# Kernel optimization log

Hardware: AMD Instinct MI355X
Metric: run time of the kernel (lower is better)

The kernel has to match this reference:

```python
import jax, jax.numpy as jnp
import numpy as np

H = 256
NUM_CONVS = 4
NUM_GRAPHS = 1024
N_PER_GRAPH = 32
ORDER = 3
NUM_TYPES = 22  # len(utils.BOND_TYPES)
NUM_NOISE_LEVEL = 50
ANNEAL_POWER = 2.0


def _build_graph():
    # Chain molecules extended to order-3 neighbors (mimics extend_graph on a path graph):
    # for |i-j| in [1,ORDER]: edge_order=|i-j|, edge_type = bond type if order 1 else NUM_TYPES+order-1.
    n = N_PER_GRAPH
    i, j = np.meshgrid(np.arange(n), np.arange(n), indexing='ij')
    dist = np.abs(i - j)
    mask = (dist >= 1) & (dist <= ORDER)
    src_l, dst_l, eo = i[mask], j[mask], dist[mask]
    offs = np.arange(NUM_GRAPHS)[:, None] * n
    src = (src_l[None, :] + offs).reshape(-1)
    dst = (dst_l[None, :] + offs).reshape(-1)
    edge_order = np.tile(eo, NUM_GRAPHS)
    rng = np.random.default_rng(0)
    bond_t = rng.integers(1, 5, size=edge_order.shape)
    edge_type = np.where(edge_order == 1, bond_t, NUM_TYPES + edge_order - 1)
    node2graph = np.repeat(np.arange(NUM_GRAPHS), n)
    return src, dst, edge_type, node2graph


def setup_inputs() -> dict:
    key = jax.random.key(0)
    ks = jax.random.split(key, 24)
    src, dst, edge_type, node2graph = _build_graph()
    N, E = node2graph.shape[0], src.shape[0]
    w = lambda k, s: (jax.random.normal(k, s, jnp.float32) * 0.05)
    sigmas = jnp.asarray(np.exp(np.linspace(np.log(10.0), np.log(0.01), NUM_NOISE_LEVEL)), dtype=jnp.float32)
    return {
        'atom_type': jnp.asarray(np.random.default_rng(1).integers(0, 100, N), jnp.int32),
        'edge_index': jnp.asarray(np.stack([src, dst]), jnp.int32),
        'edge_type': jnp.asarray(edge_type, jnp.int32),
        'node2graph': jnp.asarray(node2graph, jnp.int32),
        'noise_level': jax.random.randint(ks[0], (NUM_GRAPHS,), 0, NUM_NOISE_LEVEL, jnp.int32),
        'pos': jax.random.normal(ks[1], (N, 3), jnp.float32) * 3.0,
        'd_noise': jax.random.normal(ks[2], (E, 1), jnp.float32),
        'sigmas': sigmas,
        'node_emb': w(ks[3], (100, H)), 'edge_emb': w(ks[4], (100, H)),
        'in_W1': w(ks[5], (1, H)), 'in_b1': w(ks[6], (H,)),
        'in_W2': w(ks[7], (H, H)), 'in_b2': w(ks[8], (H,)),
        'gin_W1': w(ks[9], (NUM_CONVS, H, H)), 'gin_b1': w(ks[10], (NUM_CONVS, H)),
        'gin_W2': w(ks[11], (NUM_CONVS, H, H)), 'gin_b2': w(ks[12], (NUM_CONVS, H)),
        'out_W1': w(ks[13], (2 * H, H)), 'out_b1': w(ks[14], (H,)),
        'out_W2': w(ks[15], (H, H // 2)), 'out_b2': w(ks[16], (H // 2,)),
        'out_W3': w(ks[17], (H // 2, 1)), 'out_b3': w(ks[18], (1,)),
    }


def reference(atom_type, edge_index, edge_type, node2graph, noise_level,
              pos, d_noise, sigmas, node_emb, edge_emb,
              in_W1, in_b1, in_W2, in_b2,
              gin_W1, gin_b1, gin_W2, gin_b2,
              out_W1, out_b1, out_W2, out_b2, out_W3, out_b3):
    N = pos.shape[0]
    G = noise_level.shape[0]
    row, col = edge_index[0], edge_index[1]
    edge2graph = node2graph[row]                                  # [E]
    d = jnp.linalg.norm(pos[row] - pos[col], axis=-1, keepdims=True)  # [E,1]
    used_sigmas = sigmas[noise_level][edge2graph][:, None]        # [E,1]
    perturbed_d = d + d_noise * used_sigmas
    target = -(perturbed_d - d) / used_sigmas ** 2
    # embeddings + input MLP (Linear-relu-Linear)
    node_attr = node_emb[atom_type]                               # [N,H]
    d_emb = jax.nn.relu(perturbed_d @ in_W1 + in_b1) @ in_W2 + in_b2
    edge_attr = d_emb * edge_emb[edge_type]                       # [E,H]
    # GIN with GINE convs: agg = sum_j relu(x_j + e_ij); out = MLP(x + agg); relu between convs; residual
    x = node_attr
    n_convs = gin_W1.shape[0]
    for k in range(n_convs):
        msg = jax.nn.relu(x[row] + edge_attr)                     # [E,H]
        agg = jax.ops.segment_sum(msg, col, num_segments=N)       # [N,H]
        h = jax.nn.relu((x + agg) @ gin_W1[k] + gin_b1[k]) @ gin_W2[k] + gin_b2[k]
        if k < n_convs - 1:
            h = jax.nn.relu(h)
        x = h + x  # short_cut
    # edge score head
    feat = jnp.concatenate([x[row] * x[col], edge_attr], axis=-1)  # [E,2H]
    s = jax.nn.relu(feat @ out_W1 + out_b1)
    s = jax.nn.relu(s @ out_W2 + out_b2)
    s = s @ out_W3 + out_b3                                       # [E,1]
    scores = (s / used_sigmas).reshape(-1)
    t = target.reshape(-1)
    loss_e = 0.5 * (scores - t) ** 2 * used_sigmas.reshape(-1) ** ANNEAL_POWER
    return jax.ops.segment_sum(loss_e, edge2graph, num_segments=G)  # [G]
```

## Files before the change

### kernel.cpp

```cpp
#include <hip/hip_runtime.h>
#include <math.h>

typedef unsigned int u32;
typedef __attribute__((ext_vector_type(8))) short bf16x8;
typedef __attribute__((ext_vector_type(4))) float f32x4;

#define MFMA16(a,b,c) __builtin_amdgcn_mfma_f32_16x16x32_bf16(a,b,c,0,0,0)

__device__ inline u32 bf16r(float x){
  u32 u = __float_as_uint(x);
  return (u + 0x7fffu + ((u >> 16) & 1u)) >> 16;
}
__device__ inline u32 pack2(float a, float b){ return bf16r(a) | (bf16r(b) << 16); }
__device__ inline uint4 pack8(const float* f){
  uint4 v; v.x = pack2(f[0],f[1]); v.y = pack2(f[2],f[3]);
  v.z = pack2(f[4],f[5]); v.w = pack2(f[6],f[7]); return v;
}
__device__ inline float bf2f(short s){ return __uint_as_float(((u32)(unsigned short)s) << 16); }

__device__ __forceinline__ void gload_lds16(const void* g, void* l){
  __builtin_amdgcn_global_load_lds((const __attribute__((address_space(1))) unsigned int*)g,
                                   (__attribute__((address_space(3))) unsigned int*)l,
                                   16, 0, 0);
}

__device__ __forceinline__ int frag_off(int f, int quad){
  return (f>>1)*64 + (f&1)*32 + ((quad ^ ((f>>1)&3))*8);
}

__device__ __forceinline__ int xg2(int g, int r){ return g ^ ((r ^ (g>>1)) & 7); }

__global__ void k_cvtAll(const float* __restrict__ inW2, const float* __restrict__ gW1,
                         const float* __restrict__ gW2, const float* __restrict__ oW1,
                         const float* __restrict__ oW2,
                         short* __restrict__ w2t, short* __restrict__ gw1t,
                         short* __restrict__ gw2t, short* __restrict__ ow1t,
                         short* __restrict__ ow2t){
  int gidx = blockIdx.x*256 + threadIdx.x;
  const float* src; short* dst; int t, K8, Nf;
  if (gidx < 8192)      { src = inW2; dst = w2t; t = gidx; K8 = 32; Nf = 256; }
  else if (gidx < 40960){ int r = gidx-8192;  int c = r>>13; t = r&8191;
                          src = gW1 + (size_t)c*65536; dst = gw1t + (size_t)c*65536; K8 = 32; Nf = 256; }
  else if (gidx < 73728){ int r = gidx-40960; int c = r>>13; t = r&8191;
                          src = gW2 + (size_t)c*65536; dst = gw2t + (size_t)c*65536; K8 = 32; Nf = 256; }
  else if (gidx < 90112){ t = gidx-73728; src = oW1; dst = ow1t; K8 = 64; Nf = 256; }
  else if (gidx < 94208){ t = gidx-90112; src = oW2; dst = ow2t; K8 = 32; Nf = 128; }
  else return;
  int f = t / K8, c = t - f*K8;
  float v[8];
  #pragma unroll
  for (int j=0;j<8;j++) v[j] = src[(size_t)(c*8+j)*Nf + f];
  ((uint4*)dst)[t] = pack8(v);
}

__global__ void k_pre(const int* __restrict__ ei, const int* __restrict__ n2g,
                      const int* __restrict__ nl, const float* __restrict__ sigmas,
                      const float* __restrict__ pos, const float* __restrict__ dn, int E,
                      float* __restrict__ pd, int* __restrict__ cnt, int* __restrict__ inlist){
  int e = blockIdx.x*256 + threadIdx.x;
  if (e >= E) return;
  int r = ei[e], c = ei[E+e];
  float sg = sigmas[nl[n2g[r]]];
  float dx = pos[3*r]-pos[3*c], dy = pos[3*r+1]-pos[3*c+1], dz = pos[3*r+2]-pos[3*c+2];
  float d = sqrtf(dx*dx + dy*dy + dz*dz);
  pd[e] = d + dn[e]*sg;
  int slot = atomicAdd(&cnt[c], 1);
  if (slot < 8) inlist[c*8 + slot] = e;
}

__global__ __launch_bounds__(256) void k_attr(
    const float* __restrict__ pd, const float* __restrict__ W1, const float* __restrict__ b1,
    const short* __restrict__ W2t, const float* __restrict__ b2,
    const int* __restrict__ etype, const float* __restrict__ eemb,
    short* __restrict__ attr, int E)
{
  int tid = threadIdx.x;
  int base = blockIdx.x*64;
  int wv = tid>>6, lane = tid&63, quad = lane>>4, l15 = lane&15;
  float pdv[4];
  #pragma unroll
  for (int nt=0;nt<4;nt++) pdv[nt] = pd[base + nt*16 + l15];
  f32x4 acc[4][4];
  #pragma unroll
  for (int mt=0;mt<4;mt++) for (int nt=0;nt<4;nt++) acc[mt][nt] = (f32x4)0.f;
  #pragma unroll
  for (int s=0; s<8; s++){
    int k0 = s*32 + quad*8;
    float4 w1a = *(const float4*)(W1 + k0), w1b = *(const float4*)(W1 + k0 + 4);
    float4 b1a = *(const float4*)(b1 + k0), b1b = *(const float4*)(b1 + k0 + 4);
    bf16x8 a[4], b[4];
    #pragma unroll
    for (int mt=0;mt<4;mt++){
      int f = (wv*4+mt)*16 + l15;
      a[mt] = *(const bf16x8*)(W2t + (size_t)f*256 + k0);
    }
    #pragma unroll
    for (int nt=0;nt<4;nt++){
      float p = pdv[nt];
      float f[8] = {fmaxf(p*w1a.x+b1a.x,0.f), fmaxf(p*w1a.y+b1a.y,0.f),
                    fmaxf(p*w1a.z+b1a.z,0.f), fmaxf(p*w1a.w+b1a.w,0.f),
                    fmaxf(p*w1b.x+b1b.x,0.f), fmaxf(p*w1b.y+b1b.y,0.f),
                    fmaxf(p*w1b.z+b1b.z,0.f), fmaxf(p*w1b.w+b1b.w,0.f)};
      uint4 u = pack8(f);
      b[nt] = *(bf16x8*)&u;
    }
    #pragma unroll
    for (int mt=0;mt<4;mt++)
      #pragma unroll
      for (int nt=0;nt<4;nt++)
        acc[mt][nt] = MFMA16(a[mt], b[nt], acc[mt][nt]);
  }
  #pragma unroll
  for (int nt=0;nt<4;nt++){
    int e = base + nt*16 + l15;
    int et = etype[e];
    #pragma unroll
    for (int mt=0;mt<4;mt++){
      int f0 = (wv*4+mt)*16 + quad*4;
      float4 bb = *(const float4*)(b2 + f0);
      float4 em = *(const float4*)(eemb + (size_t)et*256 + f0);
      float v0 = (acc[mt][nt][0]+bb.x)*em.x, v1 = (acc[mt][nt][1]+bb.y)*em.y;
      float v2 = (acc[mt][nt][2]+bb.z)*em.z, v3 = (acc[mt][nt][3]+bb.w)*em.w;
      uint2 v; v.x = pack2(v0,v1); v.y = pack2(v2,v3);
      *(uint2*)(attr + (size_t)e*256 + f0) = v;
    }
  }
}

__global__ __launch_bounds__(512,3) void k_conv4(
    const int* __restrict__ at, const float* __restrict__ nemb,
    const short* __restrict__ attrS, const int* __restrict__ ei,
    const int* __restrict__ cnt, const int* __restrict__ inlist,
    const short* __restrict__ gw1t, const float* __restrict__ gb1,
    const short* __restrict__ gw2t, const float* __restrict__ gb2,
    short* __restrict__ xF)
{
  __shared__ short xls[32*256];
  __shared__ uint4 AlsV[32*32];
  __shared__ uint4 T1V [32*32];
  short* Als = (short*)AlsV;
  short* T1  = (short*)T1V;
  int tid = threadIdx.x;
  int nbase = blockIdx.x*32;
  int wv = tid>>6, lane = tid&63, quad = lane>>4, l15 = lane&15;
  int jl = tid>>4, ch = tid&15;
  int deg;
  int eid[8], rl[8];
  {
    int j = nbase + jl;
    deg = min(cnt[j], 8);
    #pragma unroll
    for (int s=0;s<8;s++){
      int e = (s < deg) ? inlist[j*8 + s] : 0;
      eid[s] = e;
      rl[s]  = (s < deg) ? (ei[e] - nbase) : 0;
    }
  }
  {
    int a = at[nbase + jl];
    const float* src = nemb + (size_t)a*256 + ch*16;
    float f[16];
    #pragma unroll
    for (int q=0;q<4;q++){
      float4 v = *(const float4*)(src + q*4);
      f[q*4]=v.x; f[q*4+1]=v.y; f[q*4+2]=v.z; f[q*4+3]=v.w;
    }
    *(uint4*)(xls + jl*256 + xg2(ch*2,   jl)*8) = pack8(f);
    *(uint4*)(xls + jl*256 + xg2(ch*2+1, jl)*8) = pack8(f+8);
  }
  __syncthreads();
  for (int c=0; c<4; c++){
    const short* W1t = gw1t + (size_t)c*65536;
    const short* W2t = gw2t + (size_t)c*65536;
    const float* b1 = gb1 + c*256;
    const float* b2 = gb2 + c*256;
    {
      float f[16];
      {
        bf16x8 v0 = *(const bf16x8*)(xls + jl*256 + xg2(ch*2,   jl)*8);
        bf16x8 v1 = *(const bf16x8*)(xls + jl*256 + xg2(ch*2+1, jl)*8);
        #pragma unroll
        for (int j=0;j<8;j++){ f[j]=bf2f(v0[j]); f[8+j]=bf2f(v1[j]); }
      }
      #pragma unroll
      for (int s=0; s<8; s++){
        if (s < deg){
          int r = rl[s];
          bf16x8 x0 = *(const bf16x8*)(xls + r*256 + xg2(ch*2,   r)*8);
          bf16x8 x1 = *(const bf16x8*)(xls + r*256 + xg2(ch*2+1, r)*8);
          const short* ar = attrS + (size_t)eid[s]*256 + ch*16;
          bf16x8 a0 = *(const bf16x8*)(ar);
          bf16x8 a1 = *(const bf16x8*)(ar + 8);
          #pragma unroll
          for (int j=0;j<8;j++){
            f[j]   += fmaxf(bf2f(x0[j]) + bf2f(a0[j]), 0.f);
            f[8+j] += fmaxf(bf2f(x1[j]) + bf2f(a1[j]), 0.f);
          }
        }
      }
      #pragma unroll
      for (int qq=0;qq<2;qq++){
        int cc = ch*2 + qq;
        *(uint4*)(Als + jl*256 + ((cc ^ (jl&7))*8)) = pack8(f + qq*8);
      }
    }
    __syncthreads();
    f32x4 acc[2][2];
    #pragma unroll
    for (int mt=0;mt<2;mt++) for (int nt=0;nt<2;nt++) acc[mt][nt] = (f32x4)0.f;
    #pragma unroll
    for (int s=0; s<8; s++){
      bf16x8 a[2], b[2];
      #pragma unroll
      for (int mt=0;mt<2;mt++)
        a[mt] = *(const bf16x8*)(W1t + (size_t)((wv*2+mt)*16 + l15)*256 + s*32 + quad*8);
      #pragma unroll
      for (int nt=0;nt<2;nt++){
        int n = nt*16 + l15; int cc = s*4 + quad;
        b[nt] = *(const bf16x8*)(Als + n*256 + ((cc ^ (n&7))*8));
      }
      #pragma unroll
      for (int mt=0;mt<2;mt++)
        #pragma unroll
        for (int nt=0;nt<2;nt++)
          acc[mt][nt] = MFMA16(a[mt], b[nt], acc[mt][nt]);
    }
    #pragma unroll
    for (int mt=0;mt<2;mt++){
      int f0 = (wv*2+mt)*16 + quad*4;
      float4 bb = *(const float4*)(b1 + f0);
      int cg = f0 >> 3, off = (quad&1)*4;
      #pragma unroll
      for (int nt=0;nt<2;nt++){
        int n = nt*16 + l15;
        float v0 = fmaxf(acc[mt][nt][0]+bb.x,0.f), v1 = fmaxf(acc[mt][nt][1]+bb.y,0.f);
        float v2 = fmaxf(acc[mt][nt][2]+bb.z,0.f), v3 = fmaxf(acc[mt][nt][3]+bb.w,0.f);
        uint2 v; v.x = pack2(v0,v1); v.y = pack2(v2,v3);
        *(uint2*)(T1 + n*256 + ((cg ^ (n&7))*8) + off) = v;
      }
    }
    __syncthreads();
    f32x4 acc2[2][2];
    #pragma unroll
    for (int mt=0;mt<2;mt++) for (int nt=0;nt<2;nt++) acc2[mt][nt] = (f32x4)0.f;
    #pragma unroll
    for (int s=0; s<8; s++){
      bf16x8 a[2], b[2];
      #pragma unroll
      for (int mt=0;mt<2;mt++)
        a[mt] = *(const bf16x8*)(W2t + (size_t)((wv*2+mt)*16 + l15)*256 + s*32 + quad*8);
      #pragma unroll
      for (int nt=0;nt<2;nt++){
        int n = nt*16 + l15; int cc = s*4 + quad;
        b[nt] = *(const bf16x8*)(T1 + n*256 + ((cc ^ (n&7))*8));
      }
      #pragma unroll
      for (int mt=0;mt<2;mt++)
        #pragma unroll
        for (int nt=0;nt<2;nt++)
          acc2[mt][nt] = MFMA16(a[mt], b[nt], acc2[mt][nt]);
    }
    #pragma unroll
    for (int mt=0;mt<2;mt++){
      int f0 = (wv*2+mt)*16 + quad*4;
      float4 bb = *(const float4*)(b2 + f0);
      int g2 = f0 >> 3, half = (quad&1)*4;
      #pragma unroll
      for (int nt=0;nt<2;nt++){
        int n = nt*16 + l15;
        short* px = xls + n*256 + xg2(g2, n)*8 + half;
        uint2 old = *(uint2*)px;
        float o0 = __uint_as_float(old.x<<16), o1 = __uint_as_float(old.x&0xffff0000u);
        float o2 = __uint_as_float(old.y<<16), o3 = __uint_as_float(old.y&0xffff0000u);
        float h0 = acc2[mt][nt][0]+bb.x, h1 = acc2[mt][nt][1]+bb.y;
        float h2 = acc2[mt][nt][2]+bb.z, h3 = acc2[mt][nt][3]+bb.w;
        if (c < 3){ h0=fmaxf(h0,0.f); h1=fmaxf(h1,0.f); h2=fmaxf(h2,0.f); h3=fmaxf(h3,0.f); }
        uint2 v; v.x = pack2(o0+h0, o1+h1); v.y = pack2(o2+h2, o3+h3);
        *(uint2*)px = v;
      }
    }
    __syncthreads();
  }
  {
    uint4 v0 = *(const uint4*)(xls + jl*256 + xg2(ch*2,   jl)*8);
    uint4 v1 = *(const uint4*)(xls + jl*256 + xg2(ch*2+1, jl)*8);
    *(uint4*)(xF + (size_t)(nbase+jl)*256 + ch*16)     = v0;
    *(uint4*)(xF + (size_t)(nbase+jl)*256 + ch*16 + 8) = v1;
  }
}

__global__ __launch_bounds__(512,2) void k_head(
    const short* __restrict__ xF, const short* __restrict__ attrS,
    const int* __restrict__ ei,
    const short* __restrict__ W1t, const float* __restrict__ ob1,
    const short* __restrict__ W2t, const float* __restrict__ ob2,
    const float* __restrict__ W3, const float* __restrict__ ob3,
    const float* __restrict__ dnoise, const int* __restrict__ n2g,
    float* __restrict__ out, int E, int G)
{
  __shared__ uint4 BlsV[16*256];
  __shared__ float Sedge[64];
  __shared__ float part[4];
  short* Bls = (short*)BlsV;
  short* T   = (short*)BlsV;
  int tid = threadIdx.x;
  int base = blockIdx.x*64;
  int wv = tid>>6, lane = tid&63, quad = lane>>4, l15 = lane&15;
  if (tid < 64) Sedge[tid] = 0.f;
  if (tid < 4) part[tid] = 0.f;
  int g8 = tid & 255, sh = tid >> 8, w4 = g8 >> 6;
  {
    int p = g8>>3, hi = (g8>>2)&1, cs = g8&3;
    int n = p*2 + hi, cc = cs ^ (p&3);
    const short* srcb = attrS + (size_t)(base+n)*256 + cc*8;
    #pragma unroll
    for (int i=0;i<4;i++){
      int s = 8 + i*2 + sh;
      gload_lds16(srcb + (s-8)*32, (char*)BlsV + (size_t)s*4096 + w4*1024);
    }
  }
  {
    int p = g8>>3, hi = (g8>>2)&1, cs = g8&3;
    int n = p*2 + hi, cc = cs ^ (p&3);
    int rr = ei[base+n], rc = ei[E+base+n];
    const short* xr = xF + (size_t)rr*256 + cc*8;
    const short* xc = xF + (size_t)rc*256 + cc*8;
    #pragma unroll
    for (int i=0;i<4;i++){
      int s = sh*4 + i;
      bf16x8 va = *(const bf16x8*)(xr + s*32);
      bf16x8 vb = *(const bf16x8*)(xc + s*32);
      float f[8];
      #pragma unroll
      for (int j=0;j<8;j++) f[j] = bf2f(va[j])*bf2f(vb[j]);
      *(uint4*)(Bls + (size_t)s*2048 + g8*8) = pack8(f);
    }
  }
  __syncthreads();
  f32x4 acc[2][4];
  #pragma unroll
  for (int mt=0;mt<2;mt++) for (int nt=0;nt<4;nt++) acc[mt][nt] = (f32x4)0.f;
  #pragma unroll
  for (int s=0; s<16; s++){
    bf16x8 a[2], b[4];
    #pragma unroll
    for (int mt=0;mt<2;mt++)
      a[mt] = *(const bf16x8*)(W1t + (size_t)((wv*2+mt)*16 + l15)*512 + s*32 + quad*8);
    #pragma unroll
    for (int nt=0;nt<4;nt++)
      b[nt] = *(const bf16x8*)(Bls + (size_t)s*2048 + frag_off(nt*16 + l15, quad));
    #pragma unroll
    for (int mt=0;mt<2;mt++)
      #pragma unroll
      for (int nt=0;nt<4;nt++)
        acc[mt][nt] = MFMA16(a[mt], b[nt], acc[mt][nt]);
  }
  __syncthreads();
  #pragma unroll
  for (int mt=0;mt<2;mt++){
    int f0 = (wv*2+mt)*16 + quad*4;
    float4 bb = *(const float4*)(ob1 + f0);
    int c = f0 >> 3, off = (quad&1)*4;
    #pragma unroll
    for (int nt=0;nt<4;nt++){
      int n = nt*16 + l15;
      float v0 = fmaxf(acc[mt][nt][0]+bb.x,0.f), v1 = fmaxf(acc[mt][nt][1]+bb.y,0.f);
      float v2 = fmaxf(acc[mt][nt][2]+bb.z,0.f), v3 = fmaxf(acc[mt][nt][3]+bb.w,0.f);
      uint2 v; v.x = pack2(v0,v1); v.y = pack2(v2,v3);
      *(uint2*)(T + n*256 + ((c ^ (n&7))*8) + off) = v;
    }
  }
  __syncthreads();
  f32x4 acc2[4];
  #pragma unroll
  for (int nt=0;nt<4;nt++) acc2[nt] = (f32x4)0.f;
  #pragma unroll
  for (int s=0; s<8; s++){
    bf16x8 a = *(const bf16x8*)(W2t + (size_t)(wv*16 + l15)*256 + s*32 + quad*8);
    #pragma unroll
    for (int nt=0;nt<4;nt++){
      int n = nt*16 + l15; int cc = s*4 + quad;
      bf16x8 b = *(const bf16x8*)(T + n*256 + ((cc ^ (n&7))*8));
      acc2[nt] = MFMA16(a, b, acc2[nt]);
    }
  }
  {
    int f0 = wv*16 + quad*4;
    float4 bb = *(const float4*)(ob2 + f0);
    float4 w3 = *(const float4*)(W3 + f0);
    #pragma unroll
    for (int nt=0;nt<4;nt++){
      float p = fmaxf(acc2[nt][0]+bb.x,0.f)*w3.x + fmaxf(acc2[nt][1]+bb.y,0.f)*w3.y
              + fmaxf(acc2[nt][2]+bb.z,0.f)*w3.z + fmaxf(acc2[nt][3]+bb.w,0.f)*w3.w;
      p += __shfl_xor(p, 16);
      p += __shfl_xor(p, 32);
      if (lane < 16) atomicAdd(&Sedge[nt*16 + l15], p);
    }
  }
  __syncthreads();
  int gbase = n2g[ei[base]];
  if (tid < 64){
    int e = base + tid;
    float sv = Sedge[tid] + ob3[0] + dnoise[e];
    float l = 0.5f*sv*sv;
    int g = n2g[ei[e]] - gbase;
    atomicAdd(&part[g & 3], l);
  }
  __syncthreads();
  if (tid < 2 && (gbase + tid) < G)
    atomicAdd(&out[gbase + tid], part[tid]);
}

static inline size_t alignup(size_t v){ return (v + 255) & ~(size_t)255; }

extern "C" void kernel_launch(void* const* d_in, const int* in_sizes, int n_in,
                              void* d_out, int out_size, void* d_ws, size_t ws_size,
                              hipStream_t stream) {
  const int*   at    = (const int*)  d_in[0];
  const int*   ei    = (const int*)  d_in[1];
  const int*   etype = (const int*)  d_in[2];
  const int*   n2g   = (const int*)  d_in[3];
  const int*   nl    = (const int*)  d_in[4];
  const float* pos   = (const float*)d_in[5];
  const float* dnoi  = (const float*)d_in[6];
  const float* sig   = (const float*)d_in[7];
  const float* nemb  = (const float*)d_in[8];
  const float* eemb  = (const float*)d_in[9];
  const float* inW1  = (const float*)d_in[10];
  const float* inb1  = (const float*)d_in[11];
  const float* inW2  = (const float*)d_in[12];
  const float* inb2  = (const float*)d_in[13];
  const float* gW1   = (const float*)d_in[14];
  const float* gb1   = (const float*)d_in[15];
  const float* gW2   = (const float*)d_in[16];
  const float* gb2   = (const float*)d_in[17];
  const float* oW1   = (const float*)d_in[18];
  const float* ob1   = (const float*)d_in[19];
  const float* oW2   = (const float*)d_in[20];
  const float* ob2   = (const float*)d_in[21];
  const float* oW3   = (const float*)d_in[22];
  const float* ob3   = (const float*)d_in[23];
  float* out = (float*)d_out;

  const int N = in_sizes[0];
  const int E = in_sizes[2];
  const int G = in_sizes[4];
  const int H = 256;

  char* w = (char*)d_ws;
  size_t off = 0;
  size_t o_attr  = off; off = alignup(off + (size_t)E*H*2);
  size_t o_xF    = off; off = alignup(off + (size_t)N*H*2);
  size_t o_pd    = off; off = alignup(off + (size_t)E*4);
  size_t o_cnt   = off; off = alignup(off + (size_t)N*4);
  size_t o_inl   = off; off = alignup(off + (size_t)N*8*4);
  size_t o_w2t   = off; off = alignup(off + (size_t)H*H*2);
  size_t o_gw1t  = off; off = alignup(off + (size_t)4*H*H*2);
  size_t o_gw2t  = off; off = alignup(off + (size_t)4*H*H*2);
  size_t o_ow1t  = off; off = alignup(off + (size_t)H*2*H*2);
  size_t o_ow2t  = off; off = alignup(off + (size_t)(H/2)*H*2);
  (void)ws_size; (void)n_in; (void)out_size;

  short* attrS = (short*)(w + o_attr);
  short* xF    = (short*)(w + o_xF);
  float* pd    = (float*)(w + o_pd);
  int*   cnt   = (int*)  (w + o_cnt);
  int*   inl   = (int*)  (w + o_inl);
  short* w2t   = (short*)(w + o_w2t);
  short* gw1t  = (short*)(w + o_gw1t);
  short* gw2t  = (short*)(w + o_gw2t);
  short* ow1t  = (short*)(w + o_ow1t);
  short* ow2t  = (short*)(w + o_ow2t);

  hipMemsetAsync(cnt, 0, (size_t)N*4, stream);
  hipMemsetAsync(out, 0, (size_t)G*4, stream);

  k_cvtAll<<<368, 256, 0, stream>>>(inW2, gW1, gW2, oW1, oW2,
                                    w2t, gw1t, gw2t, ow1t, ow2t);

  k_pre<<<(E+255)/256, 256, 0, stream>>>(ei, n2g, nl, sig, pos, dnoi, E, pd, cnt, inl);
  k_attr<<<E/64, 256, 0, stream>>>(pd, inW1, inb1, w2t, inb2, etype, eemb, attrS, E);

  k_conv4<<<G, 512, 0, stream>>>(at, nemb, attrS, ei, cnt, inl,
                                 gw1t, gb1, gw2t, gb2, xF);

  k_head<<<E/64, 512, 0, stream>>>(xF, attrS, ei, ow1t, ob1, ow2t, ob2,
                                   oW3, ob3, dnoi, n2g, out, E, G);
}
```

Baseline: 500.5 us.

## Stage each graph's edge attributes in LDS once for all four convs

The conv kernel now copies each graph's 180 edge-attribute rows (about 92KB) into shared memory at the start, using async global-to-LDS loads with an XOR swizzle. The four message-passing layers then read edge attributes from LDS instead of global memory. This removes four repeated global gathers per edge. In exchange, occupancy drops from 3 to 2 blocks per CU, the inlist buffer must be zeroed so that unused slots index valid edges, and the layout depends on exactly 180 edges per graph.

```diff
diff --git a/kernel.cpp b/kernel.cpp
--- a/kernel.cpp
+++ b/kernel.cpp
@@ -6,6 +6,7 @@
 typedef __attribute__((ext_vector_type(4))) float f32x4;
 
 #define MFMA16(a,b,c) __builtin_amdgcn_mfma_f32_16x16x32_bf16(a,b,c,0,0,0)
+#define EPG 180
 
 __device__ inline u32 bf16r(float x){
   u32 u = __float_as_uint(x);
@@ -127,7 +128,7 @@
   }
 }
 
-__global__ __launch_bounds__(512,3) void k_conv4(
+__global__ __launch_bounds__(512,2) void k_conv4(
     const int* __restrict__ at, const float* __restrict__ nemb,
     const short* __restrict__ attrS, const int* __restrict__ ei,
     const int* __restrict__ cnt, const int* __restrict__ inlist,
@@ -135,25 +136,44 @@
     const short* __restrict__ gw2t, const float* __restrict__ gb2,
     short* __restrict__ xF)
 {
+  __shared__ uint4 attrLV[EPG*32];
   __shared__ short xls[32*256];
   __shared__ uint4 AlsV[32*32];
   __shared__ uint4 T1V [32*32];
+  short* attrL = (short*)attrLV;
   short* Als = (short*)AlsV;
   short* T1  = (short*)T1V;
   int tid = threadIdx.x;
   int nbase = blockIdx.x*32;
+  int ebase = blockIdx.x*EPG;
   int wv = tid>>6, lane = tid&63, quad = lane>>4, l15 = lane&15;
   int jl = tid>>4, ch = tid&15;
-  int deg;
-  int eid[8], rl[8];
+
+  int deg, rl[8], ao0[8], ao1[8];
   {
     int j = nbase + jl;
     deg = min(cnt[j], 8);
+    int4 L0 = *(const int4*)(inlist + j*8);
+    int4 L1 = *(const int4*)(inlist + j*8 + 4);
+    int eidv[8] = {L0.x,L0.y,L0.z,L0.w,L1.x,L1.y,L1.z,L1.w};
     #pragma unroll
     for (int s=0;s<8;s++){
-      int e = (s < deg) ? inlist[j*8 + s] : 0;
-      eid[s] = e;
-      rl[s]  = (s < deg) ? (ei[e] - nbase) : 0;
+      int e = eidv[s];
+      rl[s] = ei[e] - nbase;
+      int el = e - ebase;
+      ao0[s] = el*256 + (((ch*2  ) ^ (el&7))<<3);
+      ao1[s] = el*256 + (((ch*2+1) ^ (el&7))<<3);
+    }
+  }
+  {
+    const short* asrc = attrS + (size_t)ebase*256;
+    #pragma unroll
+    for (int k=0;k<12;k++){
+      int i = tid + k*512;
+      if (k < 11 || i < EPG*32){
+        int r = i >> 5, s = i & 31;
+        gload_lds16(asrc + r*256 + ((s ^ (r&7))<<3), attrL + i*8);
+      }
     }
   }
   {
@@ -188,9 +208,8 @@
           int r = rl[s];
           bf16x8 x0 = *(const bf16x8*)(xls + r*256 + xg2(ch*2,   r)*8);
           bf16x8 x1 = *(const bf16x8*)(xls + r*256 + xg2(ch*2+1, r)*8);
-          const short* ar = attrS + (size_t)eid[s]*256 + ch*16;
-          bf16x8 a0 = *(const bf16x8*)(ar);
-          bf16x8 a1 = *(const bf16x8*)(ar + 8);
+          bf16x8 a0 = *(const bf16x8*)(attrL + ao0[s]);
+          bf16x8 a1 = *(const bf16x8*)(attrL + ao1[s]);
           #pragma unroll
           for (int j=0;j<8;j++){
             f[j]   += fmaxf(bf2f(x0[j]) + bf2f(a0[j]), 0.f);
@@ -473,6 +492,7 @@
   short* ow2t  = (short*)(w + o_ow2t);
 
   hipMemsetAsync(cnt, 0, (size_t)N*4, stream);
+  hipMemsetAsync(inl, 0, (size_t)N*8*4, stream);
   hipMemsetAsync(out, 0, (size_t)G*4, stream);
 
   k_cvtAll<<<368, 256, 0, stream>>>(inW2, gW1, gW2, oW1, oW2,
```

Measured after the change: 534.6 us. 6.8% more time.
